# Optimization experiments

Measured on AMD Instinct MI355X. Metric: run time of the kernel, lower is better.

Reference implementation:

```python
import jax, jax.numpy as jnp
import numpy as np

EPS = 1e-3
POWER = 2


def setup_inputs() -> dict:
    key = jax.random.key(0)
    k1, k2, k3 = jax.random.split(key, 3)
    inputs = jax.random.normal(k1, (8192, 512), dtype=jnp.float32)
    keys = jax.random.normal(k2, (4096, 512), dtype=jnp.float32)
    values = jax.random.normal(k3, (4096, 1000), dtype=jnp.float32)
    return {"inputs": inputs, "keys": keys, "values": values}


def reference(inputs, keys, values):
    # x: [B, D]; keys: [P, D]; values: [P, C]
    x = inputs.reshape(inputs.shape[0], -1)
    k = keys.reshape(keys.shape[0], -1)
    sq = (
        jnp.sum(x * x, axis=1, keepdims=True)
        + jnp.sum(k * k, axis=1)[None, :]
        - 2.0 * (x @ k.T)
    )
    d = jnp.sqrt(jnp.maximum(sq, 0.0))  # torch.cdist (p=2)
    dist = EPS + d ** POWER
    attn = 1.0 / dist
    attn = attn / jnp.sum(attn, axis=1, keepdims=True)
    logits = attn @ values  # [B, C]
    return logits
```

## Files before the change

### kernel.cpp

```cpp
#include <hip/hip_runtime.h>
#include <stdint.h>

#define EPS_F 1e-3f

#define NB 8192
#define NP 4096
#define ND 512
#define NC 1000
#define NCP 1024

#define SXK 21.8966f
#define INV_SXK2 (1.0f / (SXK * SXK))
#define C2DOT (2.0f * INV_SXK2)
#define SA 72571.43f
#define INV_SA (1.0f / SA)
#define SV (127.0f / 4.7f)
#define INV_SV (4.7f / 127.0f)
#define OUTC (INV_SA * INV_SV)

typedef __attribute__((ext_vector_type(4))) int intx4;

static __device__ __forceinline__ void gl_lds16(const void* g, void* l) {
  __builtin_amdgcn_global_load_lds(
      (const __attribute__((address_space(1))) void*)g,
      (__attribute__((address_space(3))) void*)l,
      16, 0, 0);
}

static __device__ __forceinline__ signed char q8(float x, float s) {
  float v = fminf(fmaxf(x * s, -127.0f), 127.0f);
  return (signed char)__float2int_rn(v);
}

#define WVM3 asm volatile("s_waitcnt vmcnt(3)" ::: "memory")
#define WVM0 asm volatile("s_waitcnt vmcnt(0)" ::: "memory")
#define LGKM0 asm volatile("s_waitcnt lgkmcnt(0)" ::: "memory")
#define SBAR0 __builtin_amdgcn_sched_barrier(0)


__global__ __launch_bounds__(256) void prep_kernel(
    const float* __restrict__ X, const float* __restrict__ Kk,
    const float* __restrict__ V,
    signed char* __restrict__ Xq, signed char* __restrict__ Kq,
    signed char* __restrict__ Vtq,
    float* __restrict__ xnorm, float* __restrict__ knorm,
    float* __restrict__ rowsum) {
  const int b = blockIdx.x;
  const int tid = threadIdx.x;
  __shared__ float tile[64][17];

  if (b < 3072) {
    const float* src;
    signed char* dst;
    float* nrm;
    int rbase;
    if (b < 2048) {
      src = X; dst = Xq; nrm = xnorm; rbase = b * 4;
      if (tid < 4) rowsum[b * 4 + tid] = 0.0f;
    } else {
      src = Kk; dst = Kq; nrm = knorm; rbase = (b - 2048) * 4;
    }
    const int w = tid >> 6, l = tid & 63;
    const int r = rbase + w;
    const float* p = src + (size_t)r * ND + l * 8;
    float4 v0 = *(const float4*)p;
    float4 v1 = *(const float4*)(p + 4);
    float s = v0.x * v0.x + v0.y * v0.y + v0.z * v0.z + v0.w * v0.w +
              v1.x * v1.x + v1.y * v1.y + v1.z * v1.z + v1.w * v1.w;
    union { signed char c[8]; uint2 u; } pk;
    pk.c[0] = q8(v0.x, SXK); pk.c[1] = q8(v0.y, SXK);
    pk.c[2] = q8(v0.z, SXK); pk.c[3] = q8(v0.w, SXK);
    pk.c[4] = q8(v1.x, SXK); pk.c[5] = q8(v1.y, SXK);
    pk.c[6] = q8(v1.z, SXK); pk.c[7] = q8(v1.w, SXK);
    *(uint2*)(dst + (size_t)r * ND + l * 8) = pk.u;
    for (int off = 32; off > 0; off >>= 1) s += __shfl_xor(s, off, 64);
    if (l == 0) nrm[r] = s;
  } else {
    const int t = b - 3072;
    const int pt = t & 63, ct = t >> 6;
    const int p0 = pt * 64, c0 = ct * 16;
    const int pl = tid >> 2, cf = (tid & 3) * 4;
    const float* vp = V + (size_t)(p0 + pl) * NC;
    for (int u = 0; u < 4; ++u) {
      int c = c0 + cf + u;
      tile[pl][cf + u] = (c < NC) ? vp[c] : 0.0f;
    }
    __syncthreads();
    const int cl = tid & 15, l = tid >> 4;
    const int c = c0 + cl;
    unsigned pk = 0;
    for (int u = 0; u < 4; ++u) {
      signed char bq = q8(tile[16 * u + l][cl], SV);
      pk |= ((unsigned)(unsigned char)bq) << (8 * u);
    }
    *(unsigned*)(Vtq + (size_t)c * NP + p0 + 4 * l) = pk;
  }
}

template <int KD>
static __device__ __forceinline__ void gemm_core_i8(
    const signed char* __restrict__ gA, const signed char* __restrict__ gB,
    signed char* lA, signed char* lB, intx4 (&acc)[4][4]) {
  const int tid = threadIdx.x;
  const int w = tid >> 6, lane = tid & 63;
  const int wm = w >> 1, wn = w & 1;
  const int lm = lane & 15, q = lane >> 4;
  const int frow = lane >> 3;
  const int fch = lane & 7;
  const int rsw = lm & 7;

  for (int k0 = 0; k0 < KD; k0 += 128) {
    for (int t = 0; t < 4; ++t) {
      const int row0 = w * 32 + t * 8;
      const int row = row0 + frow;
      const int lc = fch ^ (row & 7);
      gl_lds16(gA + (size_t)row * KD + k0 + lc * 16, &lA[row0 * 128]);
      gl_lds16(gB + (size_t)row * KD + k0 + lc * 16, &lB[row0 * 128]);
    }
    __syncthreads();
    for (int u = 0; u < 2; ++u) {
      intx4 af[4], bf[4];
      const int ch = ((u << 2) | q);
      for (int t = 0; t < 4; ++t) {
        const int ra = wm * 64 + t * 16 + lm;
        af[t] = *(const intx4*)&lA[ra * 128 + (ch ^ rsw) * 16];
        const int rb = wn * 64 + t * 16 + lm;
        bf[t] = *(const intx4*)&lB[rb * 128 + (ch ^ rsw) * 16];
      }
      for (int i = 0; i < 4; ++i)
        for (int j = 0; j < 4; ++j)
          acc[i][j] = __builtin_amdgcn_mfma_i32_16x16x64_i8(af[i], bf[j],
                                                            acc[i][j], 0, 0, 0);
    }
    __syncthreads();
  }
}

__global__ __launch_bounds__(256, 4) void gemm1_kernel(
    const signed char* __restrict__ A, const signed char* __restrict__ B,
    const float* __restrict__ xnorm, const float* __restrict__ knorm,
    signed char* __restrict__ attnq, float* __restrict__ rowsum) {
  __shared__ __align__(16) signed char lA[128 * 128];
  __shared__ __align__(16) signed char lB[128 * 128];
  const int tid = threadIdx.x;
  const int w = tid >> 6, lane = tid & 63;
  const int wm = w >> 1, wn = w & 1;
  const int lm = lane & 15, q = lane >> 4;
  const int bm = blockIdx.y * 128, bn = blockIdx.x * 128;

  intx4 acc[4][4];
  for (int i = 0; i < 4; ++i)
    for (int j = 0; j < 4; ++j) acc[i][j] = (intx4)(0);

  gemm_core_i8<ND>(A + (size_t)bm * ND, B + (size_t)bn * ND, lA, lB, acc);

  float kn[4];
  for (int j = 0; j < 4; ++j) kn[j] = knorm[bn + wn * 64 + j * 16 + lm];

  for (int i = 0; i < 4; ++i) {
    for (int r = 0; r < 4; ++r) {
      const int grow = bm + wm * 64 + i * 16 + q * 4 + r;
      const float xne = xnorm[grow] + EPS_F;
      float rs = 0.0f;
      unsigned pk = 0;
      for (int j = 0; j < 4; ++j) {
        float t = fmaf((float)acc[i][j][r], -C2DOT, xne + kn[j]);
        t = fmaxf(t, EPS_F);
        float a = __builtin_amdgcn_rcpf(t);
        rs += a;
        unsigned bq = (unsigned)__float2int_rn(fminf(a * SA, 127.0f));
        pk |= bq << (8 * j);
      }
      *(unsigned*)(attnq + (size_t)grow * NP + bn + wn * 64 + 4 * lm) = pk;
      rs += __shfl_xor(rs, 1, 16);
      rs += __shfl_xor(rs, 2, 16);
      rs += __shfl_xor(rs, 4, 16);
      rs += __shfl_xor(rs, 8, 16);
      if (lm == 0) atomicAdd(&rowsum[grow], rs);
    }
  }
}

__global__ __launch_bounds__(512, 2) void gemm2_kernel(
    const signed char* __restrict__ A, const signed char* __restrict__ B,
    const float* __restrict__ rowsum, float* __restrict__ out) {
  extern __shared__ signed char lds[];
  const int tid = threadIdx.x;
  const int w = tid >> 6, lane = tid & 63;
  const int wm = w >> 1, wn = w & 1;
  const int lm = lane & 15, q = lane >> 4;
  const int frow = lane >> 2;
  const int fgc = (lane & 3) ^ ((lane >> 3) & 3);
  const int rsw = q ^ ((lm >> 1) & 3);
  const int id = blockIdx.x;
  const int bm = (id & 31) * 256;
  const int bn = (id >> 5) * 128;

  const signed char* gAr = A + (size_t)(bm + w * 32 + frow) * NP + fgc * 16;
  const signed char* gBr = B + (size_t)(bn + w * 16 + frow) * NP + fgc * 16;
  const int aoff = (wm * 64 + lm) * 64 + rsw * 16;
  const int boff = (wn * 64 + lm) * 64 + rsw * 16;

  intx4 acc[4][4];
#pragma unroll
  for (int i = 0; i < 4; ++i)
#pragma unroll
    for (int j = 0; j < 4; ++j) acc[i][j] = (intx4)(0);

#define G2_STA(KT, SB)                                                  \
  {                                                                     \
    signed char* d = lds + (SB) + w * 2048;                             \
    gl_lds16(gAr + (size_t)(KT) * 64, d);                               \
    gl_lds16(gAr + 16 * (size_t)NP + (size_t)(KT) * 64, d + 1024);      \
  }
#define G2_STB(KT, SB)                                                  \
  {                                                                     \
    signed char* d = lds + (SB) + 16384 + w * 1024;                     \
    gl_lds16(gBr + (size_t)(KT) * 64, d);                               \
  }
#define G2_KT(KT, CB, SB, STG, WV)                                      \
  {                                                                     \
    WV;                                                                 \
    SBAR0;                                                              \
    __builtin_amdgcn_s_barrier();                                       \
    SBAR0;                                                              \
    const signed char* cA = lds + (CB);                                 \
    const signed char* cB = lds + (CB) + 16384;                         \
    intx4 af[2], bf[4];                                                 \
    _Pragma("unroll") for (int i = 0; i < 2; ++i)                       \
        af[i] = *(const intx4*)(cA + aoff + i * 1024);                  \
    _Pragma("unroll") for (int j = 0; j < 4; ++j)                       \
        bf[j] = *(const intx4*)(cB + boff + j * 1024);                  \
    if (STG) G2_STA((KT) + 2, SB);                                      \
    LGKM0;                                                              \
    SBAR0;                                                              \
    __builtin_amdgcn_s_setprio(1);                                      \
    _Pragma("unroll") for (int i = 0; i < 2; ++i)                       \
        _Pragma("unroll") for (int j = 0; j < 4; ++j)                   \
            acc[i][j] = __builtin_amdgcn_mfma_i32_16x16x64_i8(          \
                af[i], bf[j], acc[i][j], 0, 0, 0);                      \
    __builtin_amdgcn_s_setprio(0);                                      \
    _Pragma("unroll") for (int i = 0; i < 2; ++i)                       \
        af[i] = *(const intx4*)(cA + aoff + (2 + i) * 1024);            \
    if (STG) G2_STB((KT) + 2, SB);                                      \
    LGKM0;                                                              \
    SBAR0;                                                              \
    __builtin_amdgcn_s_setprio(1);                                      \
    _Pragma("unroll") for (int i = 0; i < 2; ++i)                       \
        _Pragma("unroll") for (int j = 0; j < 4; ++j)                   \
            acc[2 + i][j] = __builtin_amdgcn_mfma_i32_16x16x64_i8(      \
                af[i], bf[j], acc[2 + i][j], 0, 0, 0);                  \
    __builtin_amdgcn_s_setprio(0);                                      \
  }

  G2_STA(0, 0); G2_STB(0, 0);
  G2_STA(1, 24576); G2_STB(1, 24576);
  for (int c4 = 0; c4 < 60; c4 += 4) {
    G2_KT(c4 + 0, 0,     49152, 1, WVM3)
    G2_KT(c4 + 1, 24576, 73728, 1, WVM3)
    G2_KT(c4 + 2, 49152, 0,     1, WVM3)
    G2_KT(c4 + 3, 73728, 24576, 1, WVM3)
  }
  G2_KT(60, 0,     49152, 1, WVM3)
  G2_KT(61, 24576, 73728, 1, WVM3)
  G2_KT(62, 49152, 0,     0, WVM3)
  G2_KT(63, 73728, 0,     0, WVM0)
#undef G2_KT
#undef G2_STA
#undef G2_STB

#pragma unroll
  for (int i = 0; i < 4; ++i) {
#pragma unroll
    for (int r = 0; r < 4; ++r) {
      const int grow = bm + wm * 64 + i * 16 + q * 4 + r;
      const float inv = __builtin_amdgcn_rcpf(rowsum[grow]) * OUTC;
#pragma unroll
      for (int j = 0; j < 4; ++j) {
        const int gcol = bn + wn * 64 + j * 16 + lm;
        if (gcol < NC)
          out[(size_t)grow * NC + gcol] = (float)acc[i][j][r] * inv;
      }
    }
  }
}

extern "C" void kernel_launch(void* const* d_in, const int* in_sizes, int n_in,
                              void* d_out, int out_size, void* d_ws,
                              size_t ws_size, hipStream_t stream) {
  const float* X = (const float*)d_in[0];
  const float* Kk = (const float*)d_in[1];
  const float* V = (const float*)d_in[2];
  float* out = (float*)d_out;
  char* ws = (char*)d_ws;

  signed char* Xq = (signed char*)(ws + 0);
  signed char* Kq = (signed char*)(ws + 4194304);
  signed char* Vtq = (signed char*)(ws + 6291456);
  signed char* attnq = (signed char*)(ws + 10485760);
  float* xnorm = (float*)(ws + 44040192);
  float* knorm = (float*)(ws + 44072960);
  float* rowsum = (float*)(ws + 44089344);

  prep_kernel<<<7168, 256, 0, stream>>>(X, Kk, V, Xq, Kq, Vtq, xnorm, knorm,
                                        rowsum);
  gemm1_kernel<<<dim3(NP / 128, NB / 128), 256, 0, stream>>>(Xq, Kq, xnorm,
                                                             knorm, attnq,
                                                             rowsum);
  gemm2_kernel<<<256, 512, 98304, stream>>>(attnq, Vtq, rowsum, out);
}
```

Baseline: 179.0 us.

## Move V transpose-quantize into gemm1 launch and swizzle gemm1 block order

The V quantize/transpose work moves out of the prep kernel and into extra blocks of the gemm1 launch, so it runs alongside the GEMM tiles instead of delaying them. gemm1 now uses a 1D grid with a remapped tile index that groups blocks across the XCDs for better cache locality. Shared memory becomes a single buffer that both roles reuse. The risk is that the V blocks are scheduled after the GEMM blocks and sit on the tail, and that the remapping changes L2 reuse patterns.

```diff
diff --git a/kernel.cpp b/kernel.cpp
--- a/kernel.cpp
+++ b/kernel.cpp
@@ -38,63 +38,39 @@
 #define SBAR0 __builtin_amdgcn_sched_barrier(0)
 
 
-__global__ __launch_bounds__(256) void prep_kernel(
+__global__ __launch_bounds__(256) void prep_xk_kernel(
     const float* __restrict__ X, const float* __restrict__ Kk,
-    const float* __restrict__ V,
     signed char* __restrict__ Xq, signed char* __restrict__ Kq,
-    signed char* __restrict__ Vtq,
     float* __restrict__ xnorm, float* __restrict__ knorm,
     float* __restrict__ rowsum) {
   const int b = blockIdx.x;
   const int tid = threadIdx.x;
-  __shared__ float tile[64][17];
-
-  if (b < 3072) {
-    const float* src;
-    signed char* dst;
-    float* nrm;
-    int rbase;
-    if (b < 2048) {
-      src = X; dst = Xq; nrm = xnorm; rbase = b * 4;
-      if (tid < 4) rowsum[b * 4 + tid] = 0.0f;
-    } else {
-      src = Kk; dst = Kq; nrm = knorm; rbase = (b - 2048) * 4;
-    }
-    const int w = tid >> 6, l = tid & 63;
-    const int r = rbase + w;
-    const float* p = src + (size_t)r * ND + l * 8;
-    float4 v0 = *(const float4*)p;
-    float4 v1 = *(const float4*)(p + 4);
-    float s = v0.x * v0.x + v0.y * v0.y + v0.z * v0.z + v0.w * v0.w +
-              v1.x * v1.x + v1.y * v1.y + v1.z * v1.z + v1.w * v1.w;
-    union { signed char c[8]; uint2 u; } pk;
-    pk.c[0] = q8(v0.x, SXK); pk.c[1] = q8(v0.y, SXK);
-    pk.c[2] = q8(v0.z, SXK); pk.c[3] = q8(v0.w, SXK);
-    pk.c[4] = q8(v1.x, SXK); pk.c[5] = q8(v1.y, SXK);
-    pk.c[6] = q8(v1.z, SXK); pk.c[7] = q8(v1.w, SXK);
-    *(uint2*)(dst + (size_t)r * ND + l * 8) = pk.u;
-    for (int off = 32; off > 0; off >>= 1) s += __shfl_xor(s, off, 64);
-    if (l == 0) nrm[r] = s;
+
+  const float* src;
+  signed char* dst;
+  float* nrm;
+  int rbase;
+  if (b < 2048) {
+    src = X; dst = Xq; nrm = xnorm; rbase = b * 4;
+    if (tid < 4) rowsum[b * 4 + tid] = 0.0f;
   } else {
-    const int t = b - 3072;
-    const int pt = t & 63, ct = t >> 6;
-    const int p0 = pt * 64, c0 = ct * 16;
-    const int pl = tid >> 2, cf = (tid & 3) * 4;
-    const float* vp = V + (size_t)(p0 + pl) * NC;
-    for (int u = 0; u < 4; ++u) {
-      int c = c0 + cf + u;
-      tile[pl][cf + u] = (c < NC) ? vp[c] : 0.0f;
-    }
-    __syncthreads();
-    const int cl = tid & 15, l = tid >> 4;
-    const int c = c0 + cl;
-    unsigned pk = 0;
-    for (int u = 0; u < 4; ++u) {
-      signed char bq = q8(tile[16 * u + l][cl], SV);
-      pk |= ((unsigned)(unsigned char)bq) << (8 * u);
-    }
-    *(unsigned*)(Vtq + (size_t)c * NP + p0 + 4 * l) = pk;
-  }
+    src = Kk; dst = Kq; nrm = knorm; rbase = (b - 2048) * 4;
+  }
+  const int w = tid >> 6, l = tid & 63;
+  const int r = rbase + w;
+  const float* p = src + (size_t)r * ND + l * 8;
+  float4 v0 = *(const float4*)p;
+  float4 v1 = *(const float4*)(p + 4);
+  float s = v0.x * v0.x + v0.y * v0.y + v0.z * v0.z + v0.w * v0.w +
+            v1.x * v1.x + v1.y * v1.y + v1.z * v1.z + v1.w * v1.w;
+  union { signed char c[8]; uint2 u; } pk;
+  pk.c[0] = q8(v0.x, SXK); pk.c[1] = q8(v0.y, SXK);
+  pk.c[2] = q8(v0.z, SXK); pk.c[3] = q8(v0.w, SXK);
+  pk.c[4] = q8(v1.x, SXK); pk.c[5] = q8(v1.y, SXK);
+  pk.c[6] = q8(v1.z, SXK); pk.c[7] = q8(v1.w, SXK);
+  *(uint2*)(dst + (size_t)r * ND + l * 8) = pk.u;
+  for (int off = 32; off > 0; off >>= 1) s += __shfl_xor(s, off, 64);
+  if (l == 0) nrm[r] = s;
 }
 
 template <int KD>
@@ -138,15 +114,45 @@
 
 __global__ __launch_bounds__(256, 4) void gemm1_kernel(
     const signed char* __restrict__ A, const signed char* __restrict__ B,
+    const float* __restrict__ V,
     const float* __restrict__ xnorm, const float* __restrict__ knorm,
-    signed char* __restrict__ attnq, float* __restrict__ rowsum) {
-  __shared__ __align__(16) signed char lA[128 * 128];
-  __shared__ __align__(16) signed char lB[128 * 128];
+    signed char* __restrict__ attnq, signed char* __restrict__ Vtq,
+    float* __restrict__ rowsum) {
+  __shared__ __align__(16) signed char smem[32768];
+  const int id = blockIdx.x;
   const int tid = threadIdx.x;
+
+  if (id >= 2048) {
+    float* tile = (float*)smem;
+    const int t = id - 2048;
+    const int pt = t & 63, ct = t >> 6;
+    const int p0 = pt * 64, c0 = ct * 16;
+    const int pl = tid >> 2, cf = (tid & 3) * 4;
+    const float* vp = V + (size_t)(p0 + pl) * NC;
+    for (int u = 0; u < 4; ++u) {
+      int c = c0 + cf + u;
+      tile[pl * 17 + cf + u] = (c < NC) ? vp[c] : 0.0f;
+    }
+    __syncthreads();
+    const int cl = tid & 15, l = tid >> 4;
+    const int c = c0 + cl;
+    unsigned pk = 0;
+    for (int u = 0; u < 4; ++u) {
+      signed char bq = q8(tile[(16 * u + l) * 17 + cl], SV);
+      pk |= ((unsigned)(unsigned char)bq) << (8 * u);
+    }
+    *(unsigned*)(Vtq + (size_t)c * NP + p0 + 4 * l) = pk;
+    return;
+  }
+
+  signed char* lA = smem;
+  signed char* lB = smem + 16384;
   const int w = tid >> 6, lane = tid & 63;
   const int wm = w >> 1, wn = w & 1;
   const int lm = lane & 15, q = lane >> 4;
-  const int bm = blockIdx.y * 128, bn = blockIdx.x * 128;
+  const int sw = (id & 7) * 256 + (id >> 3);
+  const int bm = (sw >> 5) * 128;
+  const int bn = (sw & 31) * 128;
 
   intx4 acc[4][4];
   for (int i = 0; i < 4; ++i)
@@ -302,10 +308,9 @@
   float* knorm = (float*)(ws + 44072960);
   float* rowsum = (float*)(ws + 44089344);
 
-  prep_kernel<<<7168, 256, 0, stream>>>(X, Kk, V, Xq, Kq, Vtq, xnorm, knorm,
-                                        rowsum);
-  gemm1_kernel<<<dim3(NP / 128, NB / 128), 256, 0, stream>>>(Xq, Kq, xnorm,
-                                                             knorm, attnq,
-                                                             rowsum);
+  prep_xk_kernel<<<3072, 256, 0, stream>>>(X, Kk, Xq, Kq, xnorm, knorm,
+                                           rowsum);
+  gemm1_kernel<<<6144, 256, 0, stream>>>(Xq, Kq, V, xnorm, knorm, attnq, Vtq,
+                                         rowsum);
   gemm2_kernel<<<256, 512, 98304, stream>>>(attnq, Vtq, rowsum, out);
 }
```

After: 179.5 us. About the same (+0.3%).

## Replace rowsum atomics with per-slot partials and XCD-swizzle gemm1 blocks

Applied to the files above, without the earlier changes.

gemm1 no longer does atomicAdd into a zeroed rowsum buffer. Each wave column writes its row partial sum into its own slot of a 64-slot partial buffer, and gemm2 reduces those partials into an LDS table of inverse row sums after its main loop. This removes atomic contention and the zeroing step in prep. gemm1 also moves to a 1D grid with a swizzled block index, so consecutive block IDs spread across groups of 8, meant to improve L2 locality per XCD. The cost is extra partial-buffer traffic, a 64-load reduction per row in gemm2, and a bit more LDS.

```diff
diff --git a/kernel.cpp b/kernel.cpp
--- a/kernel.cpp
+++ b/kernel.cpp
@@ -43,8 +43,7 @@
     const float* __restrict__ V,
     signed char* __restrict__ Xq, signed char* __restrict__ Kq,
     signed char* __restrict__ Vtq,
-    float* __restrict__ xnorm, float* __restrict__ knorm,
-    float* __restrict__ rowsum) {
+    float* __restrict__ xnorm, float* __restrict__ knorm) {
   const int b = blockIdx.x;
   const int tid = threadIdx.x;
   __shared__ float tile[64][17];
@@ -56,7 +55,6 @@
     int rbase;
     if (b < 2048) {
       src = X; dst = Xq; nrm = xnorm; rbase = b * 4;
-      if (tid < 4) rowsum[b * 4 + tid] = 0.0f;
     } else {
       src = Kk; dst = Kq; nrm = knorm; rbase = (b - 2048) * 4;
     }
@@ -139,14 +137,18 @@
 __global__ __launch_bounds__(256, 4) void gemm1_kernel(
     const signed char* __restrict__ A, const signed char* __restrict__ B,
     const float* __restrict__ xnorm, const float* __restrict__ knorm,
-    signed char* __restrict__ attnq, float* __restrict__ rowsum) {
+    signed char* __restrict__ attnq, float* __restrict__ rowpart) {
   __shared__ __align__(16) signed char lA[128 * 128];
   __shared__ __align__(16) signed char lB[128 * 128];
   const int tid = threadIdx.x;
   const int w = tid >> 6, lane = tid & 63;
   const int wm = w >> 1, wn = w & 1;
   const int lm = lane & 15, q = lane >> 4;
-  const int bm = blockIdx.y * 128, bn = blockIdx.x * 128;
+  const int id = blockIdx.x;
+  const int sw = (id & 7) * 256 + (id >> 3);
+  const int bm = (sw >> 5) * 128;
+  const int bn = (sw & 31) * 128;
+  const int slot = (sw & 31) * 2 + wn;
 
   intx4 acc[4][4];
   for (int i = 0; i < 4; ++i)
@@ -176,14 +178,14 @@
       rs += __shfl_xor(rs, 2, 16);
       rs += __shfl_xor(rs, 4, 16);
       rs += __shfl_xor(rs, 8, 16);
-      if (lm == 0) atomicAdd(&rowsum[grow], rs);
+      if (lm == 0) rowpart[(size_t)slot * NB + grow] = rs;
     }
   }
 }
 
 __global__ __launch_bounds__(512, 2) void gemm2_kernel(
     const signed char* __restrict__ A, const signed char* __restrict__ B,
-    const float* __restrict__ rowsum, float* __restrict__ out) {
+    const float* __restrict__ rowpart, float* __restrict__ out) {
   extern __shared__ signed char lds[];
   const int tid = threadIdx.x;
   const int w = tid >> 6, lane = tid & 63;
@@ -269,12 +271,23 @@
 #undef G2_STA
 #undef G2_STB
 
+  float* rowinv = (float*)&lds[98304];
+  if (tid < 256) {
+    float s = 0.0f;
+    const float* rp = rowpart + bm + tid;
+#pragma unroll
+    for (int k = 0; k < 64; ++k) s += rp[(size_t)k * NB];
+    rowinv[tid] = __builtin_amdgcn_rcpf(s) * OUTC;
+  }
+  __syncthreads();
+
 #pragma unroll
   for (int i = 0; i < 4; ++i) {
 #pragma unroll
     for (int r = 0; r < 4; ++r) {
-      const int grow = bm + wm * 64 + i * 16 + q * 4 + r;
-      const float inv = __builtin_amdgcn_rcpf(rowsum[grow]) * OUTC;
+      const int lrow = wm * 64 + i * 16 + q * 4 + r;
+      const int grow = bm + lrow;
+      const float inv = rowinv[lrow];
 #pragma unroll
       for (int j = 0; j < 4; ++j) {
         const int gcol = bn + wn * 64 + j * 16 + lm;
@@ -300,12 +313,10 @@
   signed char* attnq = (signed char*)(ws + 10485760);
   float* xnorm = (float*)(ws + 44040192);
   float* knorm = (float*)(ws + 44072960);
-  float* rowsum = (float*)(ws + 44089344);
-
-  prep_kernel<<<7168, 256, 0, stream>>>(X, Kk, V, Xq, Kq, Vtq, xnorm, knorm,
-                                        rowsum);
-  gemm1_kernel<<<dim3(NP / 128, NB / 128), 256, 0, stream>>>(Xq, Kq, xnorm,
-                                                             knorm, attnq,
-                                                             rowsum);
-  gemm2_kernel<<<256, 512, 98304, stream>>>(attnq, Vtq, rowsum, out);
-}
+  float* rowpart = (float*)(ws + 44089344);
+
+  prep_kernel<<<7168, 256, 0, stream>>>(X, Kk, V, Xq, Kq, Vtq, xnorm, knorm);
+  gemm1_kernel<<<2048, 256, 0, stream>>>(Xq, Kq, xnorm, knorm, attnq,
+                                         rowpart);
+  gemm2_kernel<<<256, 512, 99328, stream>>>(attnq, Vtq, rowpart, out);
+}
```

Result: no change. 180.2 us (+0.7%).
